# Kernel optimization log

Measured on AMD Instinct MI355X. Metric: run time of the kernel, lower is better.

## Reference

```python
import jax, jax.numpy as jnp
import numpy as np

N = 50000      # nodes of type 'conn'
E = 250000     # edges per edge type
NT = 3         # number of edge types
H = 3          # num_heads for hidden layers
D1, D2, DO = 64, 64, 32
IN0 = 34       # 8 + 3 + 6 + 17


def setup_inputs() -> dict:
    key = jax.random.key(0)
    ks = jax.random.split(key, 40)
    it = iter(range(40))

    def nrm(shape, scale=0.1):
        return jax.random.normal(ks[next(it)], shape, dtype=jnp.float32) * scale

    inp = {}
    inp["cat_inputs"] = jax.random.randint(ks[next(it)], (N, 3), 0, 5, dtype=jnp.int32)
    inp["cont_inputs"] = jax.random.normal(ks[next(it)], (N, 17), dtype=jnp.float32)
    inp["src"] = jax.random.randint(ks[next(it)], (NT, E), 0, N)
    inp["dst"] = jax.random.randint(ks[next(it)], (NT, E), 0, N)
    # embedding tables
    inp["emb0"] = nrm((14, 8))
    inp["emb1"] = nrm((5, 3))
    inp["emb2"] = nrm((10, 6))
    # layer 1: GATConv(34 -> 64, heads=3) per etype
    inp["W1"] = nrm((NT, IN0, H * D1))
    inp["al1"] = nrm((NT, H, D1))
    inp["ar1"] = nrm((NT, H, D1))
    inp["b1"] = nrm((NT, H * D1))
    # layer 2: GATConv(192 -> 64, heads=3) per etype
    inp["W2"] = nrm((NT, H * D1, H * D2))
    inp["al2"] = nrm((NT, H, D2))
    inp["ar2"] = nrm((NT, H, D2))
    inp["b2"] = nrm((NT, H * D2))
    # output layer: GATConv(192 -> 32, heads=1) per etype
    inp["W3"] = nrm((NT, H * D2, DO))
    inp["al3"] = nrm((NT, 1, DO))
    inp["ar3"] = nrm((NT, 1, DO))
    inp["b3"] = nrm((NT, DO))
    return inp


def _gat(x, W, al, ar, b, src_t, dst_t, heads, out):
    """DGL GATConv: linear -> per-edge LeakyReLU(0.2) attention -> edge softmax
    over incoming edges -> weighted scatter-sum -> +bias -> leaky_relu(0.01)."""
    n = x.shape[0]
    feat = (x @ W).reshape(n, heads, out)          # (N,H,D)
    el = jnp.sum(feat * al, axis=-1)               # (N,H)
    er = jnp.sum(feat * ar, axis=-1)               # (N,H)
    e = jax.nn.leaky_relu(el[src_t] + er[dst_t], 0.2)  # (E,H)
    emax = jax.ops.segment_max(e, dst_t, num_segments=n)   # (N,H), -inf for empty ok
    ee = jnp.exp(e - emax[dst_t])
    den = jax.ops.segment_sum(ee, dst_t, num_segments=n)
    alpha = ee / den[dst_t]                        # (E,H)
    msg = feat[src_t] * alpha[:, :, None]          # (E,H,D)
    rst = jax.ops.segment_sum(msg, dst_t, num_segments=n) + b.reshape(1, heads, out)
    return jax.nn.leaky_relu(rst, 0.01)            # GATConv activation=F.leaky_relu


def reference(cont_inputs, emb0, emb1, emb2,
              W1, al1, ar1, b1, W2, al2, ar2, b2, W3, al3, ar3, b3,
              cat_inputs, src, dst):
    x = jnp.concatenate([emb0[cat_inputs[:, 0]],
                         emb1[cat_inputs[:, 1]],
                         emb2[cat_inputs[:, 2]],
                         cont_inputs], axis=1)     # (N,34)

    def hetero(h, W, al, ar, b, heads, out):
        # HeteroGraphConv(aggregate='mean') over NT edge types, then flatten(1)
        outs = [_gat(h, W[t], al[t], ar[t], b[t], src[t], dst[t], heads, out)
                for t in range(NT)]
        agg = jnp.mean(jnp.stack(outs, 0), axis=0)  # (N,heads,out)
        return agg.reshape(h.shape[0], heads * out)

    h = hetero(x, W1, al1, ar1, b1, H, D1)
    h = hetero(h, W2, al2, ar2, b2, H, D2)
    h = hetero(h, W3, al3, ar3, b3, 1, DO)
    return h
```

## Files before the change

kernel.cpp:

```cpp
#include <hip/hip_runtime.h>

#define NNODES 50000
#define NEDGES 250000
#define NTYPES 3
#define SCAN_B ((NNODES + 255) / 256)

typedef __attribute__((ext_vector_type(8))) short bf16x8;
typedef __attribute__((ext_vector_type(4))) float f32x4;

__device__ __forceinline__ float lrelu(float x, float s) { return x >= 0.f ? x : s * x; }

__device__ __forceinline__ unsigned short bf16_rne(float f) {
    unsigned u = __float_as_uint(f);
    unsigned r = (u + 0x7fffu + ((u >> 16) & 1u)) >> 16;
    return (unsigned short)r;
}

__global__ void build_x_kernel(const int* __restrict__ cat, const float* __restrict__ cont,
                               const float* __restrict__ e0, const float* __restrict__ e1,
                               const float* __restrict__ e2, short* __restrict__ Ahi,
                               short* __restrict__ Alo) {
    int n = blockIdx.x * 4 + (threadIdx.x >> 6);
    int k = threadIdx.x & 63;
    if (n >= NNODES) return;
    float v = 0.f;
    if (k < 8) v = e0[cat[n * 3 + 0] * 8 + k];
    else if (k < 11) v = e1[cat[n * 3 + 1] * 3 + (k - 8)];
    else if (k < 17) v = e2[cat[n * 3 + 2] * 6 + (k - 11)];
    else if (k < 34) v = cont[n * 17 + (k - 17)];
    unsigned short h = bf16_rne(v);
    float fh = __uint_as_float(((unsigned)h) << 16);
    unsigned short l = bf16_rne(v - fh);
    Ahi[(size_t)n * 64 + k] = (short)h;
    Alo[(size_t)n * 64 + k] = (short)l;
}

__global__ void hist_kernel(const int* __restrict__ dst, int* __restrict__ deg) {
    int idx = blockIdx.x * blockDim.x + threadIdx.x;
    if (idx >= NTYPES * NEDGES) return;
    int t = idx / NEDGES;
    atomicAdd(&deg[t * NNODES + dst[idx]], 1);
}

__global__ void scan1_kernel(const int* __restrict__ deg, int* __restrict__ rowptr,
                             int* __restrict__ bsum) {
    __shared__ int sd[256];
    int t = blockIdx.y, b = blockIdx.x, tid = threadIdx.x;
    int n = b * 256 + tid;
    int v = (n < NNODES) ? deg[t * NNODES + n] : 0;
    sd[tid] = v;
    __syncthreads();
    for (int off = 1; off < 256; off <<= 1) {
        int x = 0;
        if (tid >= off) x = sd[tid - off];
        __syncthreads();
        if (tid >= off) sd[tid] += x;
        __syncthreads();
    }
    int incl = sd[tid];
    if (n < NNODES) rowptr[(size_t)t * (NNODES + 1) + n] = incl - v;
    if (tid == 255) bsum[t * SCAN_B + b] = incl;
}

__global__ void scan2_kernel(int* __restrict__ bsum, int* __restrict__ rowptr) {
    int t = threadIdx.x;
    if (t >= NTYPES) return;
    int run = 0;
    for (int i = 0; i < SCAN_B; i++) {
        int v = bsum[t * SCAN_B + i];
        bsum[t * SCAN_B + i] = run;
        run += v;
    }
    rowptr[(size_t)t * (NNODES + 1) + NNODES] = run;
}

__global__ void scan3_kernel(const int* __restrict__ bsum, int* __restrict__ rowptr) {
    int t = blockIdx.y, b = blockIdx.x;
    int n = b * 256 + threadIdx.x;
    if (n < NNODES) rowptr[(size_t)t * (NNODES + 1) + n] += bsum[t * SCAN_B + b];
}

__global__ void scatter_kernel(const int* __restrict__ src, const int* __restrict__ dst,
                               const int* __restrict__ rowptr, int* __restrict__ cursor,
                               int* __restrict__ csrc) {
    int idx = blockIdx.x * blockDim.x + threadIdx.x;
    if (idx >= NTYPES * NEDGES) return;
    int t = idx / NEDGES;
    int s = src[idx], d = dst[idx];
    int pos = rowptr[(size_t)t * (NNODES + 1) + d] + atomicAdd(&cursor[t * NNODES + d], 1);
    csrc[(size_t)t * NEDGES + pos] = s;
}

__global__ void convert_B_kernel(const float* __restrict__ W, short* __restrict__ Bhi,
                                 short* __restrict__ Blo, int Kin, int Kout, int HD, int M) {
    int idx = blockIdx.x * blockDim.x + threadIdx.x;
    if (idx >= M * Kout) return;
    int m = idx / Kout, k = idx % Kout;
    int t = m / HD, j = m % HD;
    float a = (k < Kin) ? W[((size_t)t * Kin + k) * HD + j] : 0.f;
    unsigned short h = bf16_rne(a);
    float fh = __uint_as_float(((unsigned)h) << 16);
    unsigned short l = bf16_rne(a - fh);
    Bhi[(size_t)m * Kout + k] = (short)h;
    Blo[(size_t)m * Kout + k] = (short)l;
}

__global__ __launch_bounds__(256) void gemm_mfma_kernel(
    const short* __restrict__ AhiG, const short* __restrict__ AloG,
    const short* __restrict__ BhiG, const short* __restrict__ BloG, float* __restrict__ C,
    int N, int K, int M, int HD, size_t tstride) {
    __shared__ short AsH[128 * 40], AsL[128 * 40], BsH[128 * 40], BsL[128 * 40];
    int tid = threadIdx.x;
    int n0 = blockIdx.x * 128, m0 = blockIdx.y * 128;
    int wid = tid >> 6, lane = tid & 63;
    int wm = (wid >> 1) * 64, wn = (wid & 1) * 64;
    int lrow = lane & 15, kq = (lane >> 4) * 8;
    f32x4 acc[4][4] = {};

    for (int k0 = 0; k0 < K; k0 += 32) {
        __syncthreads();
#pragma unroll
        for (int p = 0; p < 2; p++) {
            int r = (tid >> 2) + p * 64;
            int kq2 = (tid & 3) * 8;
            bf16x8 z = {};
            bf16x8 vh = z, vl = z;
            int gr = n0 + r;
            if (gr < N) {
                size_t o = (size_t)gr * K + k0 + kq2;
                vh = *(const bf16x8*)(AhiG + o);
                vl = *(const bf16x8*)(AloG + o);
            }
            *(bf16x8*)&AsH[r * 40 + kq2] = vh;
            *(bf16x8*)&AsL[r * 40 + kq2] = vl;
            vh = z;
            vl = z;
            int gc = m0 + r;
            if (gc < M) {
                size_t o = (size_t)gc * K + k0 + kq2;
                vh = *(const bf16x8*)(BhiG + o);
                vl = *(const bf16x8*)(BloG + o);
            }
            *(bf16x8*)&BsH[r * 40 + kq2] = vh;
            *(bf16x8*)&BsL[r * 40 + kq2] = vl;
        }
        __syncthreads();
        bf16x8 ah[4], al[4], bh[4], bl[4];
#pragma unroll
        for (int f = 0; f < 4; f++) {
            int ra = (wm + f * 16 + lrow) * 40 + kq;
            ah[f] = *(const bf16x8*)&AsH[ra];
            al[f] = *(const bf16x8*)&AsL[ra];
            int rb = (wn + f * 16 + lrow) * 40 + kq;
            bh[f] = *(const bf16x8*)&BsH[rb];
            bl[f] = *(const bf16x8*)&BsL[rb];
        }
#pragma unroll
        for (int fa = 0; fa < 4; fa++)
#pragma unroll
            for (int fb = 0; fb < 4; fb++) {
                acc[fa][fb] =
                    __builtin_amdgcn_mfma_f32_16x16x32_bf16(al[fa], bh[fb], acc[fa][fb], 0, 0, 0);
                acc[fa][fb] =
                    __builtin_amdgcn_mfma_f32_16x16x32_bf16(ah[fa], bl[fb], acc[fa][fb], 0, 0, 0);
                acc[fa][fb] =
                    __builtin_amdgcn_mfma_f32_16x16x32_bf16(ah[fa], bh[fb], acc[fa][fb], 0, 0, 0);
            }
    }
#pragma unroll
    for (int fb = 0; fb < 4; fb++) {
        int gc = m0 + wn + fb * 16 + lrow;
        if (gc >= M) continue;
        int t = gc / HD, j = gc - t * HD;
        float* dst = C + (size_t)t * tstride + j;
#pragma unroll
        for (int fa = 0; fa < 4; fa++) {
            int rbase = n0 + wm + fa * 16 + (lane >> 4) * 4;
#pragma unroll
            for (int e = 0; e < 4; e++) {
                int gr = rbase + e;
                if (gr < N) dst[(size_t)gr * HD] = acc[fa][fb][e];
            }
        }
    }
}

template <int H, int D>
__global__ void el_er_kernel(const float* __restrict__ feat_all, const float* __restrict__ alw,
                             const float* __restrict__ arw, float* __restrict__ el_all,
                             float* __restrict__ er_all) {
    int idx = blockIdx.x * blockDim.x + threadIdx.x;
    if (idx >= NTYPES * NNODES * H) return;
    int t = idx / (NNODES * H);
    int rem = idx - t * NNODES * H;
    int n = rem / H, h = rem - (rem / H) * H;
    const float4* f4 = (const float4*)(feat_all + ((size_t)t * NNODES + n) * H * D + h * D);
    const float4* a4 = (const float4*)(alw + (t * H + h) * D);
    const float4* b4 = (const float4*)(arw + (t * H + h) * D);
    float sl = 0.f, sr = 0.f;
#pragma unroll
    for (int d = 0; d < D / 4; d++) {
        float4 v = f4[d], a = a4[d], b = b4[d];
        sl += v.x * a.x + v.y * a.y + v.z * a.z + v.w * a.w;
        sr += v.x * b.x + v.y * b.y + v.z * b.z + v.w * b.w;
    }
    el_all[((size_t)t * NNODES + n) * 4 + h] = sl;
    er_all[((size_t)t * NNODES + n) * 4 + h] = sr;
}

template <int H, int D, int BF16OUT>
__global__ __launch_bounds__(256) void gat_agg_kernel(
    const int* __restrict__ rowptr_all, const int* __restrict__ csrc_all,
    const float* __restrict__ el_all, const float* __restrict__ er_all,
    const float* __restrict__ feat_all, const float* __restrict__ b_all,
    float* __restrict__ fout, short* __restrict__ Ahi, short* __restrict__ Alo) {
    constexpr int HD = H * D;
    constexpr int EL = (HD + 63) / 64;
    int lane = threadIdx.x & 63;
    int node = blockIdx.x * (blockDim.x >> 6) + (threadIdx.x >> 6);
    if (node >= NNODES) return;
    float out[EL] = {};
#pragma unroll 1
    for (int t = 0; t < NTYPES; t++) {
        const int* rowptr = rowptr_all + (size_t)t * (NNODES + 1);
        const int* csrc = csrc_all + (size_t)t * NEDGES;
        const float* el = el_all + (size_t)t * NNODES * 4;
        const float* feat = feat_all + (size_t)t * NNODES * HD;
        float4 er4 = *(const float4*)(er_all + ((size_t)t * NNODES + node) * 4);
        float erd[3] = {er4.x, er4.y, er4.z};
        int rs = rowptr[node], re = rowptr[node + 1];
        float den[H] = {};
        float acc[EL] = {};
        for (int k = rs; k < re; k += 4) {
            int cnt = re - k;
            int s[4];
#pragma unroll
            for (int c = 0; c < 4; c++) s[c] = csrc[k + (c < cnt ? c : 0)];
            float w[4][H];
#pragma unroll
            for (int c = 0; c < 4; c++) {
                float4 e4 = *(const float4*)(el + (size_t)s[c] * 4);
                float ev[3] = {e4.x, e4.y, e4.z};
#pragma unroll
                for (int h = 0; h < H; h++) {
                    float e = lrelu(ev[h] + erd[h], 0.2f);
                    w[c][h] = (c < cnt) ? __expf(e) : 0.f;
                    den[h] += w[c][h];
                }
            }
#pragma unroll
            for (int c = 0; c < 4; c++) {
#pragma unroll
                for (int q = 0; q < EL; q++) {
                    int j = lane + q * 64;
                    constexpr bool full = (HD % 64 == 0);
                    float fv = (full || lane < HD % 64 || q < EL - 1)
                                   ? feat[(size_t)s[c] * HD + j]
                                   : 0.f;
                    int hh = (D == 64) ? q : 0;
                    acc[q] = fmaf(w[c][hh], fv, acc[q]);
                }
            }
        }
        float inv[H];
#pragma unroll
        for (int h = 0; h < H; h++) inv[h] = (re > rs) ? __frcp_rn(den[h]) : 0.f;
#pragma unroll
        for (int q = 0; q < EL; q++) {
            int j = lane + q * 64;
            if (HD % 64 == 0 || j < HD) {
                int hh = (D == 64) ? q : 0;
                float v = acc[q] * inv[hh];
                v = lrelu(v + b_all[t * HD + j], 0.01f);
                out[q] += v * (1.f / 3.f);
            }
        }
    }
#pragma unroll
    for (int q = 0; q < EL; q++) {
        int j = lane + q * 64;
        if (HD % 64 == 0 || j < HD) {
            if (BF16OUT) {
                unsigned short h = bf16_rne(out[q]);
                float fh = __uint_as_float(((unsigned)h) << 16);
                unsigned short l = bf16_rne(out[q] - fh);
                Ahi[(size_t)node * HD + j] = (short)h;
                Alo[(size_t)node * HD + j] = (short)l;
            } else {
                fout[(size_t)node * HD + j] = out[q];
            }
        }
    }
}

extern "C" void kernel_launch(void* const* d_in, const int* in_sizes, int n_in, void* d_out,
                              int out_size, void* d_ws, size_t ws_size, hipStream_t stream) {
    const int* cat = (const int*)d_in[0];
    const float* cont = (const float*)d_in[1];
    const int* src = (const int*)d_in[2];
    const int* dst = (const int*)d_in[3];
    const float* emb0 = (const float*)d_in[4];
    const float* emb1 = (const float*)d_in[5];
    const float* emb2 = (const float*)d_in[6];
    const float* W1 = (const float*)d_in[7];
    const float* al1 = (const float*)d_in[8];
    const float* ar1 = (const float*)d_in[9];
    const float* b1 = (const float*)d_in[10];
    const float* W2 = (const float*)d_in[11];
    const float* al2 = (const float*)d_in[12];
    const float* ar2 = (const float*)d_in[13];
    const float* b2 = (const float*)d_in[14];
    const float* W3 = (const float*)d_in[15];
    const float* al3 = (const float*)d_in[16];
    const float* ar3 = (const float*)d_in[17];
    const float* b3 = (const float*)d_in[18];

    float* ws = (float*)d_ws;
    float* feat_all = ws;
    short* Ahi = (short*)(feat_all + (size_t)3 * NNODES * 192);
    short* Alo = Ahi + (size_t)NNODES * 192;
    short* Bhi = Alo + (size_t)NNODES * 192;
    short* Blo = Bhi + 576 * 192;
    float* el_all = (float*)(Blo + 576 * 192);
    float* er_all = el_all + (size_t)3 * NNODES * 4;
    int* rowptr = (int*)(er_all + (size_t)3 * NNODES * 4);
    int* csrc = rowptr + NTYPES * (NNODES + 1);
    int* deg = csrc + NTYPES * NEDGES;
    int* cursor = deg + NTYPES * NNODES;
    int* bsum = cursor + NTYPES * NNODES;

    hipMemsetAsync(deg, 0, (size_t)NTYPES * NNODES * 4, stream);
    hipMemsetAsync(cursor, 0, (size_t)NTYPES * NNODES * 4, stream);
    hist_kernel<<<(NTYPES * NEDGES + 255) / 256, 256, 0, stream>>>(dst, deg);
    scan1_kernel<<<dim3(SCAN_B, NTYPES), 256, 0, stream>>>(deg, rowptr, bsum);
    scan2_kernel<<<1, 64, 0, stream>>>(bsum, rowptr);
    scan3_kernel<<<dim3(SCAN_B, NTYPES), 256, 0, stream>>>(bsum, rowptr);
    scatter_kernel<<<(NTYPES * NEDGES + 255) / 256, 256, 0, stream>>>(src, dst, rowptr, cursor,
                                                                      csrc);

    build_x_kernel<<<(NNODES + 3) / 4, 256, 0, stream>>>(cat, cont, emb0, emb1, emb2, Ahi, Alo);

    const int gx = (NNODES + 127) / 128;
    const int aggb = (NNODES + 3) / 4;

    convert_B_kernel<<<(576 * 64 + 255) / 256, 256, 0, stream>>>(W1, Bhi, Blo, 34, 64, 192, 576);
    gemm_mfma_kernel<<<dim3(gx, 5), 256, 0, stream>>>(Ahi, Alo, Bhi, Blo, feat_all, NNODES, 64, 576,
                                                      192, (size_t)NNODES * 192);
    el_er_kernel<3, 64><<<(NTYPES * NNODES * 3 + 255) / 256, 256, 0, stream>>>(feat_all, al1, ar1,
                                                                               el_all, er_all);
    gat_agg_kernel<3, 64, 1><<<aggb, 256, 0, stream>>>(rowptr, csrc, el_all, er_all, feat_all, b1,
                                                       nullptr, Ahi, Alo);

    convert_B_kernel<<<(576 * 192 + 255) / 256, 256, 0, stream>>>(W2, Bhi, Blo, 192, 192, 192, 576);
    gemm_mfma_kernel<<<dim3(gx, 5), 256, 0, stream>>>(Ahi, Alo, Bhi, Blo, feat_all, NNODES, 192,
                                                      576, 192, (size_t)NNODES * 192);
    el_er_kernel<3, 64><<<(NTYPES * NNODES * 3 + 255) / 256, 256, 0, stream>>>(feat_all, al2, ar2,
                                                                               el_all, er_all);
    gat_agg_kernel<3, 64, 1><<<aggb, 256, 0, stream>>>(rowptr, csrc, el_all, er_all, feat_all, b2,
                                                       nullptr, Ahi, Alo);

    convert_B_kernel<<<(96 * 192 + 255) / 256, 256, 0, stream>>>(W3, Bhi, Blo, 192, 192, 32, 96);
    gemm_mfma_kernel<<<dim3(gx, 1), 256, 0, stream>>>(Ahi, Alo, Bhi, Blo, feat_all, NNODES, 192, 96,
                                                      32, (size_t)NNODES * 32);
    el_er_kernel<1, 32><<<(NTYPES * NNODES * 1 + 255) / 256, 256, 0, stream>>>(feat_all, al3, ar3,
                                                                               el_all, er_all);
    gat_agg_kernel<1, 32, 0><<<aggb, 256, 0, stream>>>(rowptr, csrc, el_all, er_all, feat_all, b3,
                                                       (float*)d_out, nullptr, nullptr);
}
```

Before: 570.3 us.

## Fold attention projections into GEMM, store features as bf16, precompute edge alphas

Appends extra GEMM output columns holding W·al and W·ar, so el/er come out of the main GEMM and the separate el_er pass is dropped. Features are now stored as bf16 rather than fp32, halving gather traffic in aggregation. A new per-node kernel computes normalized edge softmax weights once, so the aggregation kernel only does a weighted gather. This costs precision on the features, extra alpha buffer writes and reads, and a serial per-thread loop over edges.

```diff
diff --git a/kernel.cpp b/kernel.cpp
--- a/kernel.cpp
+++ b/kernel.cpp
@@ -14,6 +14,9 @@
     unsigned u = __float_as_uint(f);
     unsigned r = (u + 0x7fffu + ((u >> 16) & 1u)) >> 16;
     return (unsigned short)r;
+}
+__device__ __forceinline__ float bf16_to_f(unsigned short h) {
+    return __uint_as_float((unsigned)h << 16);
 }
 
 __global__ void build_x_kernel(const int* __restrict__ cat, const float* __restrict__ cont,
@@ -29,7 +32,7 @@
     else if (k < 17) v = e2[cat[n * 3 + 2] * 6 + (k - 11)];
     else if (k < 34) v = cont[n * 17 + (k - 17)];
     unsigned short h = bf16_rne(v);
-    float fh = __uint_as_float(((unsigned)h) << 16);
+    float fh = bf16_to_f(h);
     unsigned short l = bf16_rne(v - fh);
     Ahi[(size_t)n * 64 + k] = (short)h;
     Alo[(size_t)n * 64 + k] = (short)l;
@@ -92,23 +95,47 @@
 }
 
 __global__ void convert_B_kernel(const float* __restrict__ W, short* __restrict__ Bhi,
-                                 short* __restrict__ Blo, int Kin, int Kout, int HD, int M) {
+                                 short* __restrict__ Blo, int Kin, int Kout, int HD, int Mfeat) {
     int idx = blockIdx.x * blockDim.x + threadIdx.x;
-    if (idx >= M * Kout) return;
+    if (idx >= Mfeat * Kout) return;
     int m = idx / Kout, k = idx % Kout;
     int t = m / HD, j = m % HD;
     float a = (k < Kin) ? W[((size_t)t * Kin + k) * HD + j] : 0.f;
     unsigned short h = bf16_rne(a);
-    float fh = __uint_as_float(((unsigned)h) << 16);
+    float fh = bf16_to_f(h);
     unsigned short l = bf16_rne(a - fh);
     Bhi[(size_t)m * Kout + k] = (short)h;
     Blo[(size_t)m * Kout + k] = (short)l;
 }
 
+__global__ void convert_Bel_kernel(const float* __restrict__ W, const float* __restrict__ alw,
+                                   const float* __restrict__ arw, short* __restrict__ Bhi,
+                                   short* __restrict__ Blo, int Kin, int Kout, int H, int D,
+                                   int Mfeat) {
+    int idx = blockIdx.x * blockDim.x + threadIdx.x;
+    if (idx >= 24 * Kout) return;
+    int m = idx / Kout, k = idx % Kout;
+    int t = m >> 3, r = m & 7;
+    int h = r & 3;
+    float v = 0.f;
+    if (h < H && k < Kin) {
+        const float* a = ((r >= 4) ? arw : alw) + ((size_t)t * H + h) * D;
+        const float* w = W + ((size_t)t * Kin + k) * (H * D) + h * D;
+        for (int j = 0; j < D; j++) v += w[j] * a[j];
+    }
+    unsigned short hh = bf16_rne(v);
+    float fh = bf16_to_f(hh);
+    unsigned short ll = bf16_rne(v - fh);
+    size_t o = (size_t)(Mfeat + m) * Kout + k;
+    Bhi[o] = (short)hh;
+    Blo[o] = (short)ll;
+}
+
 __global__ __launch_bounds__(256) void gemm_mfma_kernel(
     const short* __restrict__ AhiG, const short* __restrict__ AloG,
-    const short* __restrict__ BhiG, const short* __restrict__ BloG, float* __restrict__ C,
-    int N, int K, int M, int HD, size_t tstride) {
+    const short* __restrict__ BhiG, const short* __restrict__ BloG,
+    unsigned short* __restrict__ feat, float* __restrict__ elr, int N, int K, int M, int Mfeat,
+    int HD, size_t tstride) {
     __shared__ short AsH[128 * 40], AsL[128 * 40], BsH[128 * 40], BsL[128 * 40];
     int tid = threadIdx.x;
     int n0 = blockIdx.x * 128, m0 = blockIdx.y * 128;
@@ -171,107 +198,118 @@
     for (int fb = 0; fb < 4; fb++) {
         int gc = m0 + wn + fb * 16 + lrow;
         if (gc >= M) continue;
-        int t = gc / HD, j = gc - t * HD;
-        float* dst = C + (size_t)t * tstride + j;
 #pragma unroll
         for (int fa = 0; fa < 4; fa++) {
             int rbase = n0 + wm + fa * 16 + (lane >> 4) * 4;
 #pragma unroll
             for (int e = 0; e < 4; e++) {
                 int gr = rbase + e;
-                if (gr < N) dst[(size_t)gr * HD] = acc[fa][fb][e];
-            }
-        }
-    }
-}
-
-template <int H, int D>
-__global__ void el_er_kernel(const float* __restrict__ feat_all, const float* __restrict__ alw,
-                             const float* __restrict__ arw, float* __restrict__ el_all,
-                             float* __restrict__ er_all) {
+                if (gr >= N) continue;
+                float v = acc[fa][fb][e];
+                if (gc < Mfeat) {
+                    int t = gc / HD, j = gc - t * HD;
+                    feat[(size_t)t * tstride + (size_t)gr * HD + j] = bf16_rne(v);
+                } else {
+                    int m = gc - Mfeat;
+                    int t = m >> 3, r = m & 7;
+                    elr[((size_t)t * N + gr) * 8 + r] = v;
+                }
+            }
+        }
+    }
+}
+
+template <int H>
+__global__ void alpha_kernel(const int* __restrict__ rowptr_all, const int* __restrict__ csrc_all,
+                             const float* __restrict__ elr, float* __restrict__ alpha_all) {
     int idx = blockIdx.x * blockDim.x + threadIdx.x;
-    if (idx >= NTYPES * NNODES * H) return;
-    int t = idx / (NNODES * H);
-    int rem = idx - t * NNODES * H;
-    int n = rem / H, h = rem - (rem / H) * H;
-    const float4* f4 = (const float4*)(feat_all + ((size_t)t * NNODES + n) * H * D + h * D);
-    const float4* a4 = (const float4*)(alw + (t * H + h) * D);
-    const float4* b4 = (const float4*)(arw + (t * H + h) * D);
-    float sl = 0.f, sr = 0.f;
-#pragma unroll
-    for (int d = 0; d < D / 4; d++) {
-        float4 v = f4[d], a = a4[d], b = b4[d];
-        sl += v.x * a.x + v.y * a.y + v.z * a.z + v.w * a.w;
-        sr += v.x * b.x + v.y * b.y + v.z * b.z + v.w * b.w;
-    }
-    el_all[((size_t)t * NNODES + n) * 4 + h] = sl;
-    er_all[((size_t)t * NNODES + n) * 4 + h] = sr;
+    if (idx >= NTYPES * NNODES) return;
+    int t = idx / NNODES, node = idx - t * NNODES;
+    const int* rowptr = rowptr_all + t * (NNODES + 1);
+    const int* csrc = csrc_all + (size_t)t * NEDGES;
+    const float* elr_t = elr + (size_t)t * NNODES * 8;
+    float4* alpha4 = (float4*)(alpha_all + (size_t)t * NEDGES * 4);
+    float4 er4 = *(const float4*)(elr_t + (size_t)node * 8 + 4);
+    float erd[3] = {er4.x, er4.y, er4.z};
+    int rs = rowptr[node], re = rowptr[node + 1];
+    float den[H];
+#pragma unroll
+    for (int h = 0; h < H; h++) den[h] = 0.f;
+    for (int k = rs; k < re; k++) {
+        int s = csrc[k];
+        float4 e4 = *(const float4*)(elr_t + (size_t)s * 8);
+        float ev[3] = {e4.x, e4.y, e4.z};
+        float w[4] = {0.f, 0.f, 0.f, 0.f};
+#pragma unroll
+        for (int h = 0; h < H; h++) {
+            w[h] = __expf(lrelu(ev[h] + erd[h], 0.2f));
+            den[h] += w[h];
+        }
+        alpha4[k] = (float4){w[0], w[1], w[2], w[3]};
+    }
+    float inv[H];
+#pragma unroll
+    for (int h = 0; h < H; h++) inv[h] = __frcp_rn(den[h]);
+    for (int k = rs; k < re; k++) {
+        float4 w = alpha4[k];
+        w.x *= inv[0];
+        if (H > 1) {
+            w.y *= inv[1];
+            w.z *= inv[2];
+        }
+        alpha4[k] = w;
+    }
 }
 
 template <int H, int D, int BF16OUT>
 __global__ __launch_bounds__(256) void gat_agg_kernel(
     const int* __restrict__ rowptr_all, const int* __restrict__ csrc_all,
-    const float* __restrict__ el_all, const float* __restrict__ er_all,
-    const float* __restrict__ feat_all, const float* __restrict__ b_all,
-    float* __restrict__ fout, short* __restrict__ Ahi, short* __restrict__ Alo) {
+    const float* __restrict__ alpha_all, const unsigned short* __restrict__ feat_all,
+    const float* __restrict__ b_all, float* __restrict__ fout, short* __restrict__ Ahi,
+    short* __restrict__ Alo) {
     constexpr int HD = H * D;
     constexpr int EL = (HD + 63) / 64;
     int lane = threadIdx.x & 63;
-    int node = blockIdx.x * (blockDim.x >> 6) + (threadIdx.x >> 6);
+    int node = blockIdx.x * 4 + (threadIdx.x >> 6);
     if (node >= NNODES) return;
     float out[EL] = {};
 #pragma unroll 1
     for (int t = 0; t < NTYPES; t++) {
-        const int* rowptr = rowptr_all + (size_t)t * (NNODES + 1);
+        const int* rowptr = rowptr_all + t * (NNODES + 1);
         const int* csrc = csrc_all + (size_t)t * NEDGES;
-        const float* el = el_all + (size_t)t * NNODES * 4;
-        const float* feat = feat_all + (size_t)t * NNODES * HD;
-        float4 er4 = *(const float4*)(er_all + ((size_t)t * NNODES + node) * 4);
-        float erd[3] = {er4.x, er4.y, er4.z};
+        const float4* alpha4 = (const float4*)(alpha_all + (size_t)t * NEDGES * 4);
+        const unsigned short* feat = feat_all + (size_t)t * NNODES * HD;
         int rs = rowptr[node], re = rowptr[node + 1];
-        float den[H] = {};
         float acc[EL] = {};
         for (int k = rs; k < re; k += 4) {
             int cnt = re - k;
             int s[4];
-#pragma unroll
-            for (int c = 0; c < 4; c++) s[c] = csrc[k + (c < cnt ? c : 0)];
-            float w[4][H];
+            float4 w4[4];
 #pragma unroll
             for (int c = 0; c < 4; c++) {
-                float4 e4 = *(const float4*)(el + (size_t)s[c] * 4);
-                float ev[3] = {e4.x, e4.y, e4.z};
-#pragma unroll
-                for (int h = 0; h < H; h++) {
-                    float e = lrelu(ev[h] + erd[h], 0.2f);
-                    w[c][h] = (c < cnt) ? __expf(e) : 0.f;
-                    den[h] += w[c][h];
-                }
+                s[c] = csrc[k + (c < cnt ? c : 0)];
+                w4[c] = (c < cnt) ? alpha4[k + c] : (float4){0.f, 0.f, 0.f, 0.f};
             }
 #pragma unroll
             for (int c = 0; c < 4; c++) {
+                float wv[3] = {w4[c].x, w4[c].y, w4[c].z};
 #pragma unroll
                 for (int q = 0; q < EL; q++) {
                     int j = lane + q * 64;
                     constexpr bool full = (HD % 64 == 0);
-                    float fv = (full || lane < HD % 64 || q < EL - 1)
-                                   ? feat[(size_t)s[c] * HD + j]
-                                   : 0.f;
+                    float fv = 0.f;
+                    if (full || lane < (HD % 64) || q < EL - 1)
+                        fv = bf16_to_f(feat[(size_t)s[c] * HD + j]);
                     int hh = (D == 64) ? q : 0;
-                    acc[q] = fmaf(w[c][hh], fv, acc[q]);
+                    acc[q] = fmaf(wv[hh], fv, acc[q]);
                 }
             }
         }
-        float inv[H];
-#pragma unroll
-        for (int h = 0; h < H; h++) inv[h] = (re > rs) ? __frcp_rn(den[h]) : 0.f;
 #pragma unroll
         for (int q = 0; q < EL; q++) {
             int j = lane + q * 64;
             if (HD % 64 == 0 || j < HD) {
-                int hh = (D == 64) ? q : 0;
-                float v = acc[q] * inv[hh];
-                v = lrelu(v + b_all[t * HD + j], 0.01f);
+                float v = lrelu(acc[q] + b_all[t * HD + j], 0.01f);
                 out[q] += v * (1.f / 3.f);
             }
         }
@@ -282,7 +320,7 @@
         if (HD % 64 == 0 || j < HD) {
             if (BF16OUT) {
                 unsigned short h = bf16_rne(out[q]);
-                float fh = __uint_as_float(((unsigned)h) << 16);
+                float fh = bf16_to_f(h);
                 unsigned short l = bf16_rne(out[q] - fh);
                 Ahi[(size_t)node * HD + j] = (short)h;
                 Alo[(size_t)node * HD + j] = (short)l;
@@ -315,15 +353,14 @@
     const float* ar3 = (const float*)d_in[17];
     const float* b3 = (const float*)d_in[18];
 
-    float* ws = (float*)d_ws;
-    float* feat_all = ws;
+    unsigned short* feat_all = (unsigned short*)d_ws;
     short* Ahi = (short*)(feat_all + (size_t)3 * NNODES * 192);
     short* Alo = Ahi + (size_t)NNODES * 192;
     short* Bhi = Alo + (size_t)NNODES * 192;
-    short* Blo = Bhi + 576 * 192;
-    float* el_all = (float*)(Blo + 576 * 192);
-    float* er_all = el_all + (size_t)3 * NNODES * 4;
-    int* rowptr = (int*)(er_all + (size_t)3 * NNODES * 4);
+    short* Blo = Bhi + 600 * 192;
+    float* elr = (float*)(Blo + 600 * 192);
+    float* alpha_all = elr + (size_t)3 * NNODES * 8;
+    int* rowptr = (int*)(alpha_all + (size_t)3 * NEDGES * 4);
     int* csrc = rowptr + NTYPES * (NNODES + 1);
     int* deg = csrc + NTYPES * NEDGES;
     int* cursor = deg + NTYPES * NNODES;
@@ -342,28 +379,32 @@
 
     const int gx = (NNODES + 127) / 128;
     const int aggb = (NNODES + 3) / 4;
+    const int nb = (NTYPES * NNODES + 255) / 256;
 
     convert_B_kernel<<<(576 * 64 + 255) / 256, 256, 0, stream>>>(W1, Bhi, Blo, 34, 64, 192, 576);
-    gemm_mfma_kernel<<<dim3(gx, 5), 256, 0, stream>>>(Ahi, Alo, Bhi, Blo, feat_all, NNODES, 64, 576,
-                                                      192, (size_t)NNODES * 192);
-    el_er_kernel<3, 64><<<(NTYPES * NNODES * 3 + 255) / 256, 256, 0, stream>>>(feat_all, al1, ar1,
-                                                                               el_all, er_all);
-    gat_agg_kernel<3, 64, 1><<<aggb, 256, 0, stream>>>(rowptr, csrc, el_all, er_all, feat_all, b1,
+    convert_Bel_kernel<<<(24 * 64 + 255) / 256, 256, 0, stream>>>(W1, al1, ar1, Bhi, Blo, 34, 64, 3,
+                                                                  64, 576);
+    gemm_mfma_kernel<<<dim3(gx, 5), 256, 0, stream>>>(Ahi, Alo, Bhi, Blo, feat_all, elr, NNODES, 64,
+                                                      600, 576, 192, (size_t)NNODES * 192);
+    alpha_kernel<3><<<nb, 256, 0, stream>>>(rowptr, csrc, elr, alpha_all);
+    gat_agg_kernel<3, 64, 1><<<aggb, 256, 0, stream>>>(rowptr, csrc, alpha_all, feat_all, b1,
                                                        nullptr, Ahi, Alo);
 
     convert_B_kernel<<<(576 * 192 + 255) / 256, 256, 0, stream>>>(W2, Bhi, Blo, 192, 192, 192, 576);
-    gemm_mfma_kernel<<<dim3(gx, 5), 256, 0, stream>>>(Ahi, Alo, Bhi, Blo, feat_all, NNODES, 192,
-                                                      576, 192, (size_t)NNODES * 192);
-    el_er_kernel<3, 64><<<(NTYPES * NNODES * 3 + 255) / 256, 256, 0, stream>>>(feat_all, al2, ar2,
-                                                                               el_all, er_all);
-    gat_agg_kernel<3, 64, 1><<<aggb, 256, 0, stream>>>(rowptr, csrc, el_all, er_all, feat_all, b2,
+    convert_Bel_kernel<<<(24 * 192 + 255) / 256, 256, 0, stream>>>(W2, al2, ar2, Bhi, Blo, 192, 192,
+                                                                   3, 64, 576);
+    gemm_mfma_kernel<<<dim3(gx, 5), 256, 0, stream>>>(Ahi, Alo, Bhi, Blo, feat_all, elr, NNODES,
+                                                      192, 600, 576, 192, (size_t)NNODES * 192);
+    alpha_kernel<3><<<nb, 256, 0, stream>>>(rowptr, csrc, elr, alpha_all);
+    gat_agg_kernel<3, 64, 1><<<aggb, 256, 0, stream>>>(rowptr, csrc, alpha_all, feat_all, b2,
                                                        nullptr, Ahi, Alo);
 
     convert_B_kernel<<<(96 * 192 + 255) / 256, 256, 0, stream>>>(W3, Bhi, Blo, 192, 192, 32, 96);
-    gemm_mfma_kernel<<<dim3(gx, 1), 256, 0, stream>>>(Ahi, Alo, Bhi, Blo, feat_all, NNODES, 192, 96,
-                                                      32, (size_t)NNODES * 32);
-    el_er_kernel<1, 32><<<(NTYPES * NNODES * 1 + 255) / 256, 256, 0, stream>>>(feat_all, al3, ar3,
-                                                                               el_all, er_all);
-    gat_agg_kernel<1, 32, 0><<<aggb, 256, 0, stream>>>(rowptr, csrc, el_all, er_all, feat_all, b3,
+    convert_Bel_kernel<<<(24 * 192 + 255) / 256, 256, 0, stream>>>(W3, al3, ar3, Bhi, Blo, 192, 192,
+                                                                   1, 32, 96);
+    gemm_mfma_kernel<<<dim3(gx, 1), 256, 0, stream>>>(Ahi, Alo, Bhi, Blo, feat_all, elr, NNODES,
+                                                      192, 120, 96, 32, (size_t)NNODES * 32);
+    alpha_kernel<1><<<nb, 256, 0, stream>>>(rowptr, csrc, elr, alpha_all);
+    gat_agg_kernel<1, 32, 0><<<aggb, 256, 0, stream>>>(rowptr, csrc, alpha_all, feat_all, b3,
                                                        (float*)d_out, nullptr, nullptr);
 }
```

New measurement: 583.3 us. 2.3% more time.
